# Optimization experiments

Hardware: AMD Instinct MI355X
Metric: run time of the kernel (lower is better)

The kernel has to match this reference:

```python
import jax, jax.numpy as jnp
import numpy as np

B, S, D, H = 2, 1024, 512, 8  # batch, seq, per-head dim (=in_dim), n_heads
NEG_INF = -1e30  # matches torch -inf after exp underflow, grad-safe


def _linear_init(key, fan_in, fan_out, bias=True):
    kw, kb = jax.random.split(key)
    bound = 1.0 / np.sqrt(fan_in)
    W = jax.random.uniform(kw, (fan_in, fan_out), jnp.float32, -bound, bound)
    if not bias:
        return W
    b = jax.random.uniform(kb, (fan_out,), jnp.float32, -bound, bound)
    return W, b


def setup_inputs() -> dict:
    key = jax.random.key(0)
    ks = jax.random.split(key, 8)
    x = jax.random.normal(ks[0], (B, S, D), jnp.float32)
    y = jax.random.normal(ks[1], (B, S, D), jnp.float32)
    Wq, bq = _linear_init(ks[2], D, H * D)          # query: Linear(in_dim, out_dim*H)
    Wk, bk = _linear_init(ks[3], D, H * D)          # key
    Wv, bv = _linear_init(ks[4], D, H * D)          # value
    Wp = _linear_init(ks[5], D, D, bias=False)      # projection: Linear(y_in_dim, y_out_dim//H, bias=False)
    gamma = jax.random.uniform(ks[6], (H, 1, 1, 1), jnp.float32) + 0.001
    mask = jax.random.bernoulli(ks[7], 0.95, (S,))  # True = keep column
    return dict(x=x, y=y, Wq=Wq, bq=bq, Wk=Wk, bk=bk, Wv=Wv, bv=bv, Wp=Wp,
                gamma=gamma, mask=mask)


def reference(x, y, Wq, bq, Wk, bk, Wv, bv, Wp, gamma, mask):
    b, s, _ = x.shape
    h = gamma.shape[0]
    # projections, then head-major split (split_cat along feature dim -> batch dim)
    q = (x @ Wq + bq).reshape(b, s, h, -1).transpose(2, 0, 1, 3)  # (h,B,S,d)
    k = (y @ Wk + bk).reshape(b, s, h, -1).transpose(2, 0, 1, 3)  # (h,B,S,d)
    v = (y @ Wv + bv).reshape(b, s, h, -1).transpose(2, 0, 1, 3)  # (h,B,S,dv)
    # energy = bmm(q, k^T)  (no scaling in the original)
    energy = jnp.einsum('hbsd,hbtd->hbst', q, k)                  # (h,B,S,S)
    # boolean column mask: energy[..., ~mask] = -inf
    energy = jnp.where(mask[None, None, None, :], energy, NEG_INF)
    attn = jax.nn.softmax(energy, axis=-1)
    # out = bmm(attention^T, v): out[t] = sum_s attn[s, t] * v[s]
    out = jnp.einsum('hbst,hbsv->hbtv', attn, v)                  # (h,B,S,dv)
    # gamma-weighted residual blend against projected x (broadcast over heads)
    xp = x @ Wp                                                   # (B,S,dv)
    out = (gamma * out + xp[None]) / (gamma + 1.0)                # (h,B,S,dv)
    return out.transpose(1, 0, 2, 3)                              # (B,h,S,dv)
```

## Files before the change

kernel.cpp:

```cpp
#include <hip/hip_runtime.h>
#include <stdint.h>

#define Bb 2
#define Ss 1024
#define Dd 512
#define Hh 8
#define HD 4096
#define Mm 2048

typedef _Float16 f16x8 __attribute__((ext_vector_type(8)));
typedef _Float16 f16x4 __attribute__((ext_vector_type(4)));
typedef float    f32x4 __attribute__((ext_vector_type(4)));

#define LOG2E 1.44269504f

#define GLOAD16(g, l)                                                          \
    __builtin_amdgcn_global_load_lds(                                          \
        (const __attribute__((address_space(1))) void*)(g),                    \
        (__attribute__((address_space(3))) void*)(l), 16, 0, 0)

__global__ __launch_bounds__(256) void cvt_f16(
    const float* __restrict__ in, _Float16* __restrict__ out, int n)
{
    int i = (blockIdx.x * 256 + threadIdx.x) * 4;
    if (i < n) {
        float4 u = *(const float4*)(in + i);
        f16x4 o;
        o[0] = (_Float16)u.x; o[1] = (_Float16)u.y;
        o[2] = (_Float16)u.z; o[3] = (_Float16)u.w;
        *(f16x4*)(out + i) = o;
    }
}

__global__ __launch_bounds__(256) void cvt_w_pk(
    const float* __restrict__ W, int ld, int col0,
    _Float16* __restrict__ out, int NC)
{
    const int n  = blockIdx.x * 256 + threadIdx.x;
    const int k0 = blockIdx.y * 8;
    f16x8 o;
#pragma unroll
    for (int j = 0; j < 8; j++)
        o[j] = (_Float16)W[(size_t)(k0 + j) * ld + col0 + n];
    *(f16x8*)(out + ((size_t)(k0 >> 3) * NC + n) * 8) = o;
}

__global__ __launch_bounds__(256) void stage_all(
    const float* __restrict__ x, const float* __restrict__ y,
    const float* __restrict__ Wq, const float* __restrict__ Wk,
    const float* __restrict__ Wv, const float* __restrict__ Wp,
    _Float16* __restrict__ xf, _Float16* __restrict__ yf,
    _Float16* __restrict__ Wbuf, int NCq, size_t wslot)
{
    const int f = blockIdx.x;
    if (f < 2048) {
        const float* in = (f < 1024) ? x : y;
        _Float16* out   = (f < 1024) ? xf : yf;
        const int i = ((f & 1023) * 256 + threadIdx.x) * 4;
        float4 u = *(const float4*)(in + i);
        f16x4 o;
        o[0] = (_Float16)u.x; o[1] = (_Float16)u.y;
        o[2] = (_Float16)u.z; o[3] = (_Float16)u.w;
        *(f16x4*)(out + i) = o;
        return;
    }
    int l = f - 2048;
    const float* W; int ld, NCz, z, bx, by;
    if (l < 3072) {
        z = l >> 10; l &= 1023;
        W = (z == 0) ? Wq : (z == 1) ? Wk : Wv; ld = HD; NCz = NCq;
        bx = l & 15; by = l >> 4;
    } else {
        z = 3; l -= 3072;
        W = Wp; ld = Dd; NCz = Dd;
        bx = l & 1; by = l >> 1;
    }
    const int n  = bx * 256 + threadIdx.x;
    const int k0 = by * 8;
    f16x8 o;
#pragma unroll
    for (int j = 0; j < 8; j++)
        o[j] = (_Float16)W[(size_t)(k0 + j) * ld + n];
    *(f16x8*)(Wbuf + (size_t)z * wslot + ((size_t)(k0 >> 3) * NCz + n) * 8) = o;
}

__device__ __forceinline__ void proj_body(
    const _Float16* __restrict__ A, const _Float16* __restrict__ Wpk,
    const float* __restrict__ bias, int bias0,
    _Float16* __restrict__ C, int NC, int packC, int bx, int by)
{
    __shared__ _Float16 lsA[2][4096];
    __shared__ _Float16 lsB[2][4096];
    const int t = threadIdx.x;
    const int lane = t & 63, wave = t >> 6;
    const int quad = lane >> 4, l15 = lane & 15;
    const int m0b = by * 128, n0b = bx * 128;
    const int aw = (wave >> 1) * 64, bw = (wave & 1) * 64;
    const int qx = (quad ^ ((l15 >> 2) & 3)) * 8;

    const _Float16* ag = A + (size_t)(m0b + (t >> 2)) * Dd
                           + ((t & 3) ^ ((t >> 4) & 3)) * 8;
    const _Float16* bg = Wpk + ((size_t)(t >> 7) * NC + n0b + (t & 127)) * 8;
    const size_t arj = (size_t)64 * Dd;
    const size_t bcs = (size_t)NC * 8;

    f32x4 acc[4][4] = {};
    GLOAD16(ag,           &lsA[0][t * 8]);
    GLOAD16(ag + arj,     &lsA[0][t * 8 + 2048]);
    GLOAD16(bg,           &lsB[0][t * 8]);
    GLOAD16(bg + 2 * bcs, &lsB[0][t * 8 + 2048]);
    __syncthreads();
    int cur = 0;
    for (int kb = 0; kb < Dd; kb += 32) {
        if (kb + 32 < Dd) {
            const int nb = cur ^ 1;
            GLOAD16(ag + kb + 32,       &lsA[nb][t * 8]);
            GLOAD16(ag + arj + kb + 32, &lsA[nb][t * 8 + 2048]);
            GLOAD16(bg + (size_t)((kb >> 3) + 4) * bcs, &lsB[nb][t * 8]);
            GLOAD16(bg + (size_t)((kb >> 3) + 6) * bcs, &lsB[nb][t * 8 + 2048]);
        }
        f16x8 af[4], bf[4];
#pragma unroll
        for (int mi = 0; mi < 4; mi++)
            af[mi] = *(const f16x8*)&lsA[cur][(aw + mi * 16 + l15) * 32 + qx];
#pragma unroll
        for (int ni = 0; ni < 4; ni++)
            bf[ni] = *(const f16x8*)&lsB[cur][quad * 1024 + (bw + ni * 16 + l15) * 8];
#pragma unroll
        for (int mi = 0; mi < 4; mi++)
#pragma unroll
            for (int ni = 0; ni < 4; ni++)
                acc[mi][ni] = __builtin_amdgcn_mfma_f32_16x16x32_f16(af[mi], bf[ni], acc[mi][ni], 0, 0, 0);
        __syncthreads();
        cur ^= 1;
    }

#pragma unroll
    for (int mi = 0; mi < 4; mi++) {
        const int row0 = m0b + aw + mi * 16 + quad * 4;
#pragma unroll
        for (int ni = 0; ni < 4; ni++) {
            const int col = n0b + bw + ni * 16 + l15;
            const float bv = bias ? bias[bias0 + col] : 0.0f;
            if (packC) {
                f16x4 o;
#pragma unroll
                for (int r = 0; r < 4; r++) o[r] = (_Float16)(acc[mi][ni][r] + bv);
                *(f16x4*)(C + ((size_t)(row0 >> 3) * NC + col) * 8 + (row0 & 7)) = o;
            } else {
#pragma unroll
                for (int r = 0; r < 4; r++)
                    C[(size_t)(row0 + r) * NC + col] = (_Float16)(acc[mi][ni][r] + bv);
            }
        }
    }
}

__global__ __launch_bounds__(256, 4) void proj_f16(
    const _Float16* __restrict__ A, const _Float16* __restrict__ Wpk,
    const float* __restrict__ bias, int bias0,
    _Float16* __restrict__ C, int NC, int packC)
{
    proj_body(A, Wpk, bias, bias0, C, NC, packC, blockIdx.x, blockIdx.y);
}

__global__ __launch_bounds__(256, 4) void proj_flat(
    const _Float16* __restrict__ xf, const _Float16* __restrict__ yf,
    const _Float16* __restrict__ Wpk, size_t wslot,
    const float* __restrict__ bq, const float* __restrict__ bk,
    const float* __restrict__ bv,
    _Float16* __restrict__ qb, _Float16* __restrict__ kb,
    _Float16* __restrict__ vb, _Float16* __restrict__ xp)
{
    const int f = blockIdx.x;
    int z, bx, by;
    if (f < 1536) { z = f >> 9; const int r = f & 511; bx = r & 31; by = r >> 5; }
    else         { z = 3;      const int r = f - 1536; bx = r & 3;  by = r >> 2; }
    const _Float16* A = (z == 0 || z == 3) ? xf : yf;
    const _Float16* W = Wpk + (size_t)z * wslot;
    const float* bias = (z == 0) ? bq : (z == 1) ? bk : (z == 2) ? bv : nullptr;
    _Float16* C = (z == 0) ? qb : (z == 1) ? kb : (z == 2) ? vb : xp;
    const int NCz = (z == 3) ? Dd : (Hh * Dd);
    proj_body(A, W, bias, 0, C, NCz, z == 2, bx, by);
}

__global__ __launch_bounds__(256, 4) void energy_f16(
    const _Float16* __restrict__ Q, const _Float16* __restrict__ Kb,
    const int* __restrict__ mask, _Float16* __restrict__ E,
    float* __restrict__ part, int NC)
{
    __shared__ _Float16 lsA[2][4096];
    __shared__ _Float16 lsB[2][4096];
    const int zl = blockIdx.x;
    const int b = zl & 1, hloc = zl >> 1;
    const _Float16* qz = Q + (size_t)b * Ss * NC + hloc * Dd;
    const _Float16* kz = Kb + (size_t)b * Ss * NC + hloc * Dd;
    _Float16* Ez = E + (size_t)zl * Ss * Ss;

    const int t = threadIdx.x;
    const int lane = t & 63, wave = t >> 6;
    const int quad = lane >> 4, l15 = lane & 15;
    const int sb = blockIdx.y * 128;
    const int tb = blockIdx.z * 128;
    const int sw = (wave >> 1) * 64, tw = (wave & 1) * 64;
    const int qx = (quad ^ ((l15 >> 2) & 3)) * 8;

    const int sc = ((t & 3) ^ ((t >> 4) & 3)) * 8;
    const _Float16* ag = qz + (size_t)(sb + (t >> 2)) * NC + sc;
    const _Float16* bg = kz + (size_t)(tb + (t >> 2)) * NC + sc;
    const size_t rj = (size_t)64 * NC;

    f32x4 acc[4][4] = {};
    GLOAD16(ag,      &lsA[0][t * 8]);
    GLOAD16(ag + rj, &lsA[0][t * 8 + 2048]);
    GLOAD16(bg,      &lsB[0][t * 8]);
    GLOAD16(bg + rj, &lsB[0][t * 8 + 2048]);
    __syncthreads();
    int cur = 0;
    for (int kb = 0; kb < Dd; kb += 32) {
        if (kb + 32 < Dd) {
            const int nb = cur ^ 1;
            GLOAD16(ag + kb + 32,      &lsA[nb][t * 8]);
            GLOAD16(ag + rj + kb + 32, &lsA[nb][t * 8 + 2048]);
            GLOAD16(bg + kb + 32,      &lsB[nb][t * 8]);
            GLOAD16(bg + rj + kb + 32, &lsB[nb][t * 8 + 2048]);
        }
        f16x8 af[4], bf[4];
#pragma unroll
        for (int mi = 0; mi < 4; mi++)
            af[mi] = *(const f16x8*)&lsA[cur][(sw + mi * 16 + l15) * 32 + qx];
#pragma unroll
        for (int ni = 0; ni < 4; ni++)
            bf[ni] = *(const f16x8*)&lsB[cur][(tw + ni * 16 + l15) * 32 + qx];
#pragma unroll
        for (int mi = 0; mi < 4; mi++)
#pragma unroll
            for (int ni = 0; ni < 4; ni++)
                acc[mi][ni] = __builtin_amdgcn_mfma_f32_16x16x32_f16(af[mi], bf[ni], acc[mi][ni], 0, 0, 0);
        __syncthreads();
        cur ^= 1;
    }

#pragma unroll
    for (int ni = 0; ni < 4; ni++) {
        const int tcol = tb + tw + ni * 16 + l15;
        const int keep = mask[tcol];
#pragma unroll
        for (int mi = 0; mi < 4; mi++)
#pragma unroll
            for (int r = 0; r < 4; r++) {
                const float v = keep ? acc[mi][ni][r] : -30000.0f;
                acc[mi][ni][r] = (float)(_Float16)v;
            }
    }

    const int jc = blockIdx.z * 2 + (wave & 1);
    float* ps = part + ((size_t)(zl * 16 + jc) * 1024) * 2;
#pragma unroll
    for (int mi = 0; mi < 4; mi++) {
        const int s0 = sb + sw + mi * 16 + quad * 4;
        _Float16* base = Ez + (size_t)(s0 >> 3) * (Ss * 8) + (s0 & 7);
        float m[4], l[4];
#pragma unroll
        for (int r = 0; r < 4; r++) {
            float mm = fmaxf(fmaxf(acc[mi][0][r], acc[mi][1][r]),
                             fmaxf(acc[mi][2][r], acc[mi][3][r]));
#pragma unroll
            for (int off = 1; off < 16; off <<= 1) mm = fmaxf(mm, __shfl_xor(mm, off));
            m[r] = mm;
            l[r] = 0.0f;
        }
#pragma unroll
        for (int ni = 0; ni < 4; ni++) {
            const int tcol = tb + tw + ni * 16 + l15;
            f16x4 o;
#pragma unroll
            for (int r = 0; r < 4; r++) {
                const float p = __expf(acc[mi][ni][r] - m[r]);
                l[r] += p;
                o[r] = (_Float16)p;
            }
            *(f16x4*)(base + (size_t)tcol * 8) = o;
        }
#pragma unroll
        for (int r = 0; r < 4; r++) {
            float ll = l[r];
#pragma unroll
            for (int off = 1; off < 16; off <<= 1) ll += __shfl_xor(ll, off);
            if (l15 == 0) {
                const int s = s0 + r;
                ps[s * 2]     = m[r];
                ps[s * 2 + 1] = ll;
            }
        }
    }
}

__global__ __launch_bounds__(256, 4) void pv_f16(
    const _Float16* __restrict__ Epk, const _Float16* __restrict__ Vpk,
    const _Float16* __restrict__ Xp, const float* __restrict__ G,
    const float* __restrict__ part, float* __restrict__ Out, int h0, int NC)
{
    __shared__ _Float16 lsP[2][2048];
    __shared__ _Float16 lsV[2][4096];
    __shared__ _Float16 lsS[1024];
    const int zl = blockIdx.x;
    const int b = zl & 1, hloc = zl >> 1;
    const int h = h0 + hloc;
    const _Float16* az = Epk + (size_t)zl * Ss * Ss;

    const int t = threadIdx.x;
    const int lane = t & 63, wave = t >> 6;
    const int quad = lane >> 4, l15 = lane & 15;
    const int tb = blockIdx.y * 64;
    const int cb = blockIdx.z * 128;
    const int tw = (wave >> 1) * 32, cw = (wave & 1) * 64;
    const int jc0 = blockIdx.y;

    const _Float16* pg = az + ((size_t)(t >> 6) * Ss + tb + (t & 63)) * 8;
    const _Float16* vg = Vpk + (((size_t)((b * Ss) >> 3) + (t >> 7)) * NC
                                + hloc * Dd + cb + (t & 127)) * 8;
    const size_t acs = (size_t)Ss * 8;
    const size_t vcs = (size_t)NC * 8;

    f32x4 acc[2][4] = {};
    GLOAD16(pg,           &lsP[0][t * 8]);
    GLOAD16(vg,           &lsV[0][t * 8]);
    GLOAD16(vg + 2 * vcs, &lsV[0][t * 8 + 2048]);
    {
        const float* pz = part + (size_t)zl * 16 * 1024 * 2;
        for (int ss = t; ss < 1024; ss += 256) {
            const float* p = pz + (size_t)ss * 2;
            float m = -3.4e38f;
#pragma unroll
            for (int j = 0; j < 16; j++) m = fmaxf(m, p[(size_t)j * 2048]);
            float l = 0.0f;
#pragma unroll
            for (int j = 0; j < 16; j++)
                l += p[(size_t)j * 2048 + 1] * __expf(p[(size_t)j * 2048] - m);
            const float C = m + __logf(l);
            lsS[ss] = (_Float16)__expf(p[(size_t)jc0 * 2048] - C);
        }
    }
    __syncthreads();
    int cur = 0;
    for (int kb = 0; kb < Ss; kb += 32) {
        if (kb + 32 < Ss) {
            const int nb = cur ^ 1;
            GLOAD16(pg + ((size_t)(kb >> 3) + 4) * acs, &lsP[nb][t * 8]);
            GLOAD16(vg + ((size_t)(kb >> 3) + 4) * vcs, &lsV[nb][t * 8]);
            GLOAD16(vg + ((size_t)(kb >> 3) + 6) * vcs, &lsV[nb][t * 8 + 2048]);
        }
        const f16x8 sc8 = *(const f16x8*)&lsS[kb + quad * 8];
        f16x8 af[2], bf[4];
#pragma unroll
        for (int mi = 0; mi < 2; mi++) {
            const f16x8 pu = *(const f16x8*)&lsP[cur][quad * 512 + (tw + mi * 16 + l15) * 8];
            af[mi] = pu * sc8;
        }
#pragma unroll
        for (int ni = 0; ni < 4; ni++)
            bf[ni] = *(const f16x8*)&lsV[cur][quad * 1024 + (cw + ni * 16 + l15) * 8];
#pragma unroll
        for (int mi = 0; mi < 2; mi++)
#pragma unroll
            for (int ni = 0; ni < 4; ni++)
                acc[mi][ni] = __builtin_amdgcn_mfma_f32_16x16x32_f16(af[mi], bf[ni], acc[mi][ni], 0, 0, 0);
        __syncthreads();
        cur ^= 1;
    }

    const float g = G[h];
    const float inv = 1.0f / (g + 1.0f);
#pragma unroll
    for (int mi = 0; mi < 2; mi++) {
        const int tr0 = tb + tw + mi * 16 + quad * 4;
#pragma unroll
        for (int r = 0; r < 4; r++) {
            const int tt = tr0 + r;
            const _Float16* xrow = Xp + (size_t)(b * Ss + tt) * Dd;
            float* orow = Out + ((size_t)((b * Hh + h) * Ss + tt)) * Dd;
#pragma unroll
            for (int ni = 0; ni < 4; ni++) {
                const int c = cb + cw + ni * 16 + l15;
                orow[c] = (g * acc[mi][ni][r] + (float)xrow[c]) * inv;
            }
        }
    }
}

extern "C" void kernel_launch(void* const* d_in, const int* in_sizes, int n_in,
                              void* d_out, int out_size, void* d_ws, size_t ws_size,
                              hipStream_t stream) {
    const float* x    = (const float*)d_in[0];
    const float* y    = (const float*)d_in[1];
    const float* Wq   = (const float*)d_in[2];
    const float* bq   = (const float*)d_in[3];
    const float* Wk   = (const float*)d_in[4];
    const float* bk   = (const float*)d_in[5];
    const float* Wv   = (const float*)d_in[6];
    const float* bv   = (const float*)d_in[7];
    const float* Wp   = (const float*)d_in[8];
    const float* gm   = (const float*)d_in[9];
    const int*   mask = (const int*)d_in[10];

    const int HG = (ws_size >= (size_t)134217728) ? 8 : 4;
    const int NC = HG * Dd;
    const int NZ = 2 * HG;
    const size_t wslot = (size_t)512 * NC;

    char* ws = (char*)d_ws;
    size_t off = 0;
    _Float16* Wbuf = (_Float16*)(ws + off); off += (size_t)(HG == 8 ? 4 : 1) * wslot * 2;
    _Float16* qb   = (_Float16*)(ws + off); off += (size_t)Mm * NC * 2;
    _Float16* kb   = (_Float16*)(ws + off); off += (size_t)Mm * NC * 2;
    _Float16* vb   = (_Float16*)(ws + off); off += (size_t)Mm * NC * 2;
    _Float16* xp   = (_Float16*)(ws + off); off += (size_t)Mm * Dd * 2;
    _Float16* en   = (_Float16*)(ws + off); off += (size_t)NZ * Ss * Ss * 2;
    float*    part = (float*)(ws + off);    off += (size_t)NZ * 16 * 1024 * 2 * 4;
    _Float16* xf   = en;
    _Float16* yf   = en + (size_t)Mm * 512;

    dim3 blk(256);
    const int NXY = Mm * 512;

    if (HG == 8) {
        stage_all<<<dim3(5248), blk, 0, stream>>>(x, y, Wq, Wk, Wv, Wp,
                                                  xf, yf, Wbuf, NC, wslot);
        proj_flat<<<dim3(1600), blk, 0, stream>>>(xf, yf, Wbuf, wslot,
                                                  bq, bk, bv, qb, kb, vb, xp);
        energy_f16<<<dim3(NZ, 8, 8), blk, 0, stream>>>(qb, kb, mask, en, part, NC);
        pv_f16<<<dim3(NZ, 16, 4), blk, 0, stream>>>(en, vb, xp, gm, part,
                                                    (float*)d_out, 0, NC);
    } else {
        cvt_f16<<<dim3(NXY / 1024), blk, 0, stream>>>(x, xf, NXY);
        cvt_w_pk<<<dim3(2, 64), blk, 0, stream>>>(Wp, Dd, 0, Wbuf, Dd);
        proj_f16<<<dim3(4, 16), blk, 0, stream>>>(xf, Wbuf, nullptr, 0, xp, Dd, 0);

        for (int h0 = 0; h0 < Hh; h0 += HG) {
            cvt_f16<<<dim3(NXY / 1024), blk, 0, stream>>>(x, xf, NXY);
            cvt_f16<<<dim3(NXY / 1024), blk, 0, stream>>>(y, yf, NXY);

            cvt_w_pk<<<dim3(NC / 256, 64), blk, 0, stream>>>(Wq, HD, h0 * Dd, Wbuf, NC);
            proj_f16<<<dim3(NC / 128, 16), blk, 0, stream>>>(xf, Wbuf, bq, h0 * Dd, qb, NC, 0);
            cvt_w_pk<<<dim3(NC / 256, 64), blk, 0, stream>>>(Wk, HD, h0 * Dd, Wbuf, NC);
            proj_f16<<<dim3(NC / 128, 16), blk, 0, stream>>>(yf, Wbuf, bk, h0 * Dd, kb, NC, 0);
            cvt_w_pk<<<dim3(NC / 256, 64), blk, 0, stream>>>(Wv, HD, h0 * Dd, Wbuf, NC);
            proj_f16<<<dim3(NC / 128, 16), blk, 0, stream>>>(yf, Wbuf, bv, h0 * Dd, vb, NC, 1);

            energy_f16<<<dim3(NZ, 8, 8), blk, 0, stream>>>(qb, kb, mask, en, part, NC);
            pv_f16<<<dim3(NZ, 16, 4), blk, 0, stream>>>(en, vb, xp, gm, part,
                                                        (float*)d_out, h0, NC);
        }
    }
}
```

Measured before the change: 205.2 us.

## Triple-buffer LDS loads with vmcnt-gated single barrier in GEMM kernels

Converts the projection, energy and PV GEMM loops from double-buffered global-to-LDS loads with two barriers per step to a three-stage ring buffer. Each step waits on vmcnt until the current stage's loads have landed, then issues one barrier before prefetching two stages ahead. The aim is to hide global load latency better and cut synchronisation cost. In exchange, LDS use per block grows by half and launch bounds drop from 4 to 3 blocks per CU, which lowers occupancy.

New measurement: 217.0 us. 1.06x slower.

```diff
diff --git a/kernel.cpp b/kernel.cpp
--- a/kernel.cpp
+++ b/kernel.cpp
@@ -18,6 +18,13 @@
     __builtin_amdgcn_global_load_lds(                                          \
         (const __attribute__((address_space(1))) void*)(g),                    \
         (__attribute__((address_space(3))) void*)(l), 16, 0, 0)
+
+#define WAITCNT_BAR(N)                                                         \
+    do {                                                                       \
+        asm volatile("s_waitcnt vmcnt(" #N ")" ::: "memory");                  \
+        __builtin_amdgcn_s_barrier();                                          \
+        asm volatile("" ::: "memory");                                         \
+    } while (0)
 
 __global__ __launch_bounds__(256) void cvt_f16(
     const float* __restrict__ in, _Float16* __restrict__ out, int n)
@@ -89,8 +96,8 @@
     const float* __restrict__ bias, int bias0,
     _Float16* __restrict__ C, int NC, int packC, int bx, int by)
 {
-    __shared__ _Float16 lsA[2][4096];
-    __shared__ _Float16 lsB[2][4096];
+    __shared__ _Float16 lsA[3][4096];
+    __shared__ _Float16 lsB[3][4096];
     const int t = threadIdx.x;
     const int lane = t & 63, wave = t >> 6;
     const int quad = lane >> 4, l15 = lane & 15;
@@ -104,21 +111,22 @@
     const size_t arj = (size_t)64 * Dd;
     const size_t bcs = (size_t)NC * 8;
 
+#define PSTAGE(buf, s)                                                         \
+    do {                                                                       \
+        GLOAD16(ag + (s) * 32,       &lsA[buf][t * 8]);                        \
+        GLOAD16(ag + arj + (s) * 32, &lsA[buf][t * 8 + 2048]);                 \
+        GLOAD16(bg + (size_t)(4 * (s))     * bcs, &lsB[buf][t * 8]);           \
+        GLOAD16(bg + (size_t)(4 * (s) + 2) * bcs, &lsB[buf][t * 8 + 2048]);    \
+    } while (0)
+
     f32x4 acc[4][4] = {};
-    GLOAD16(ag,           &lsA[0][t * 8]);
-    GLOAD16(ag + arj,     &lsA[0][t * 8 + 2048]);
-    GLOAD16(bg,           &lsB[0][t * 8]);
-    GLOAD16(bg + 2 * bcs, &lsB[0][t * 8 + 2048]);
-    __syncthreads();
-    int cur = 0;
-    for (int kb = 0; kb < Dd; kb += 32) {
-        if (kb + 32 < Dd) {
-            const int nb = cur ^ 1;
-            GLOAD16(ag + kb + 32,       &lsA[nb][t * 8]);
-            GLOAD16(ag + arj + kb + 32, &lsA[nb][t * 8 + 2048]);
-            GLOAD16(bg + (size_t)((kb >> 3) + 4) * bcs, &lsB[nb][t * 8]);
-            GLOAD16(bg + (size_t)((kb >> 3) + 6) * bcs, &lsB[nb][t * 8 + 2048]);
-        }
+    PSTAGE(0, 0);
+    PSTAGE(1, 1);
+    for (int s = 0; s < 16; ++s) {
+        const int cur = s % 3;
+        if (s == 15) WAITCNT_BAR(0);
+        else         WAITCNT_BAR(4);
+        if (s + 2 < 16) PSTAGE((s + 2) % 3, s + 2);
         f16x8 af[4], bf[4];
 #pragma unroll
         for (int mi = 0; mi < 4; mi++)
@@ -131,9 +139,8 @@
 #pragma unroll
             for (int ni = 0; ni < 4; ni++)
                 acc[mi][ni] = __builtin_amdgcn_mfma_f32_16x16x32_f16(af[mi], bf[ni], acc[mi][ni], 0, 0, 0);
-        __syncthreads();
-        cur ^= 1;
-    }
+    }
+#undef PSTAGE
 
 #pragma unroll
     for (int mi = 0; mi < 4; mi++) {
@@ -156,7 +163,7 @@
     }
 }
 
-__global__ __launch_bounds__(256, 4) void proj_f16(
+__global__ __launch_bounds__(256, 3) void proj_f16(
     const _Float16* __restrict__ A, const _Float16* __restrict__ Wpk,
     const float* __restrict__ bias, int bias0,
     _Float16* __restrict__ C, int NC, int packC)
@@ -164,7 +171,7 @@
     proj_body(A, Wpk, bias, bias0, C, NC, packC, blockIdx.x, blockIdx.y);
 }
 
-__global__ __launch_bounds__(256, 4) void proj_flat(
+__global__ __launch_bounds__(256, 3) void proj_flat(
     const _Float16* __restrict__ xf, const _Float16* __restrict__ yf,
     const _Float16* __restrict__ Wpk, size_t wslot,
     const float* __restrict__ bq, const float* __restrict__ bk,
@@ -184,13 +191,13 @@
     proj_body(A, W, bias, 0, C, NCz, z == 2, bx, by);
 }
 
-__global__ __launch_bounds__(256, 4) void energy_f16(
+__global__ __launch_bounds__(256, 3) void energy_f16(
     const _Float16* __restrict__ Q, const _Float16* __restrict__ Kb,
     const int* __restrict__ mask, _Float16* __restrict__ E,
     float* __restrict__ part, int NC)
 {
-    __shared__ _Float16 lsA[2][4096];
-    __shared__ _Float16 lsB[2][4096];
+    __shared__ _Float16 lsA[3][4096];
+    __shared__ _Float16 lsB[3][4096];
     const int zl = blockIdx.x;
     const int b = zl & 1, hloc = zl >> 1;
     const _Float16* qz = Q + (size_t)b * Ss * NC + hloc * Dd;
@@ -210,21 +217,22 @@
     const _Float16* bg = kz + (size_t)(tb + (t >> 2)) * NC + sc;
     const size_t rj = (size_t)64 * NC;
 
+#define ESTAGE(buf, s)                                                         \
+    do {                                                                       \
+        GLOAD16(ag + (s) * 32,      &lsA[buf][t * 8]);                         \
+        GLOAD16(ag + rj + (s) * 32, &lsA[buf][t * 8 + 2048]);                  \
+        GLOAD16(bg + (s) * 32,      &lsB[buf][t * 8]);                         \
+        GLOAD16(bg + rj + (s) * 32, &lsB[buf][t * 8 + 2048]);                  \
+    } while (0)
+
     f32x4 acc[4][4] = {};
-    GLOAD16(ag,      &lsA[0][t * 8]);
-    GLOAD16(ag + rj, &lsA[0][t * 8 + 2048]);
-    GLOAD16(bg,      &lsB[0][t * 8]);
-    GLOAD16(bg + rj, &lsB[0][t * 8 + 2048]);
-    __syncthreads();
-    int cur = 0;
-    for (int kb = 0; kb < Dd; kb += 32) {
-        if (kb + 32 < Dd) {
-            const int nb = cur ^ 1;
-            GLOAD16(ag + kb + 32,      &lsA[nb][t * 8]);
-            GLOAD16(ag + rj + kb + 32, &lsA[nb][t * 8 + 2048]);
-            GLOAD16(bg + kb + 32,      &lsB[nb][t * 8]);
-            GLOAD16(bg + rj + kb + 32, &lsB[nb][t * 8 + 2048]);
-        }
+    ESTAGE(0, 0);
+    ESTAGE(1, 1);
+    for (int s = 0; s < 16; ++s) {
+        const int cur = s % 3;
+        if (s == 15) WAITCNT_BAR(0);
+        else         WAITCNT_BAR(4);
+        if (s + 2 < 16) ESTAGE((s + 2) % 3, s + 2);
         f16x8 af[4], bf[4];
 #pragma unroll
         for (int mi = 0; mi < 4; mi++)
@@ -237,9 +245,8 @@
 #pragma unroll
             for (int ni = 0; ni < 4; ni++)
                 acc[mi][ni] = __builtin_amdgcn_mfma_f32_16x16x32_f16(af[mi], bf[ni], acc[mi][ni], 0, 0, 0);
-        __syncthreads();
-        cur ^= 1;
-    }
+    }
+#undef ESTAGE
 
 #pragma unroll
     for (int ni = 0; ni < 4; ni++) {
@@ -301,8 +308,8 @@
     const _Float16* __restrict__ Xp, const float* __restrict__ G,
     const float* __restrict__ part, float* __restrict__ Out, int h0, int NC)
 {
-    __shared__ _Float16 lsP[2][2048];
-    __shared__ _Float16 lsV[2][4096];
+    __shared__ _Float16 lsP[3][2048];
+    __shared__ _Float16 lsV[3][4096];
     __shared__ _Float16 lsS[1024];
     const int zl = blockIdx.x;
     const int b = zl & 1, hloc = zl >> 1;
@@ -323,10 +330,6 @@
     const size_t acs = (size_t)Ss * 8;
     const size_t vcs = (size_t)NC * 8;
 
-    f32x4 acc[2][4] = {};
-    GLOAD16(pg,           &lsP[0][t * 8]);
-    GLOAD16(vg,           &lsV[0][t * 8]);
-    GLOAD16(vg + 2 * vcs, &lsV[0][t * 8 + 2048]);
     {
         const float* pz = part + (size_t)zl * 16 * 1024 * 2;
         for (int ss = t; ss < 1024; ss += 256) {
@@ -343,15 +346,23 @@
         }
     }
     __syncthreads();
-    int cur = 0;
-    for (int kb = 0; kb < Ss; kb += 32) {
-        if (kb + 32 < Ss) {
-            const int nb = cur ^ 1;
-            GLOAD16(pg + ((size_t)(kb >> 3) + 4) * acs, &lsP[nb][t * 8]);
-            GLOAD16(vg + ((size_t)(kb >> 3) + 4) * vcs, &lsV[nb][t * 8]);
-            GLOAD16(vg + ((size_t)(kb >> 3) + 6) * vcs, &lsV[nb][t * 8 + 2048]);
-        }
-        const f16x8 sc8 = *(const f16x8*)&lsS[kb + quad * 8];
+
+#define VSTAGE(buf, s)                                                         \
+    do {                                                                       \
+        GLOAD16(pg + (size_t)(4 * (s))     * acs, &lsP[buf][t * 8]);           \
+        GLOAD16(vg + (size_t)(4 * (s))     * vcs, &lsV[buf][t * 8]);           \
+        GLOAD16(vg + (size_t)(4 * (s) + 2) * vcs, &lsV[buf][t * 8 + 2048]);    \
+    } while (0)
+
+    f32x4 acc[2][4] = {};
+    VSTAGE(0, 0);
+    VSTAGE(1, 1);
+    for (int s = 0; s < 32; ++s) {
+        const int cur = s % 3;
+        if (s == 31) WAITCNT_BAR(0);
+        else         WAITCNT_BAR(3);
+        if (s + 2 < 32) VSTAGE((s + 2) % 3, s + 2);
+        const f16x8 sc8 = *(const f16x8*)&lsS[s * 32 + quad * 8];
         f16x8 af[2], bf[4];
 #pragma unroll
         for (int mi = 0; mi < 2; mi++) {
@@ -366,9 +377,8 @@
 #pragma unroll
             for (int ni = 0; ni < 4; ni++)
                 acc[mi][ni] = __builtin_amdgcn_mfma_f32_16x16x32_f16(af[mi], bf[ni], acc[mi][ni], 0, 0, 0);
-        __syncthreads();
-        cur ^= 1;
-    }
+    }
+#undef VSTAGE
 
     const float g = G[h];
     const float inv = 1.0f / (g + 1.0f);
```
